# Optimization experiments

Hardware: AMD Instinct MI355X
Metric: run time of the kernel (lower is better)

The kernel has to match this reference:

```python
import jax, jax.numpy as jnp
import numpy as np

N_NODES = 50000


def gcn_conv(x, W, b, src, dst, n):
    """PyG GCNConv: add self-loops, sym-normalize, linear, scatter-add."""
    loop = jnp.arange(n, dtype=src.dtype)
    s = jnp.concatenate([src, loop])  # [E+N]
    d = jnp.concatenate([dst, loop])
    deg = jax.ops.segment_sum(jnp.ones_like(s, dtype=x.dtype), d, num_segments=n)
    dinv = jnp.where(deg > 0, jax.lax.rsqrt(deg), 0.0)  # deg^-1/2
    norm = dinv[s] * dinv[d]  # [E+N]
    h = x @ W  # [N, out] dense GEMM first (in >= out)
    msg = h[s] * norm[:, None]  # gather + scale
    out = jax.ops.segment_sum(msg, d, num_segments=n)  # scatter-add
    return out + b


def setup_inputs() -> dict:
    key = jax.random.key(0)
    k1, k2, k3, k4, k5, k6, k7, k8 = jax.random.split(key, 8)
    in_c, hid_c, out_c = 512, 128, 64
    n, e, l = N_NODES, 800000, 100000
    x = jax.random.normal(k1, (n, in_c), dtype=jnp.float32)
    edge_index = jax.random.randint(k2, (2, e), 0, n, dtype=jnp.int64)
    edge_label_index = jax.random.randint(k3, (2, l), 0, n, dtype=jnp.int64)
    # Glorot-ish init for weights, zeros for biases (PyG default bias=zeros)
    W1 = jax.random.normal(k4, (in_c, hid_c), dtype=jnp.float32) / np.sqrt(in_c)
    b1 = jnp.zeros((hid_c,), dtype=jnp.float32)
    W2 = jax.random.normal(k5, (hid_c, out_c), dtype=jnp.float32) / np.sqrt(hid_c)
    b2 = jnp.zeros((out_c,), dtype=jnp.float32)
    return {"x": x, "edge_index": edge_index, "edge_label_index": edge_label_index,
            "W1": W1, "b1": b1, "W2": W2, "b2": b2}


def reference(x, edge_index, edge_label_index, W1, b1, W2, b2):
    n = x.shape[0]
    src, dst = edge_index[0], edge_index[1]
    z = jax.nn.relu(gcn_conv(x, W1, b1, src, dst, n))
    z = gcn_conv(z, W2, b2, src, dst, n)
    es, ed = edge_label_index[0], edge_label_index[1]
    return jnp.sum(z[es] * z[ed], axis=-1).reshape(-1)
```

## Files before the change

kernel.cpp:

```cpp
#include <hip/hip_runtime.h>

#define IN_C  512
#define HID_C 128
#define OUT_C 64

using short8 = __attribute__((ext_vector_type(8))) short;
using floatx4 = __attribute__((ext_vector_type(4))) float;

__device__ inline unsigned short f2bf(float f) {
    unsigned u = __builtin_bit_cast(unsigned, f);
    u += 0x7FFFu + ((u >> 16) & 1u);
    return (unsigned short)(u >> 16);
}
__device__ inline float bf2f(unsigned short h) {
    unsigned u = ((unsigned)h) << 16;
    return __builtin_bit_cast(float, u);
}

__global__ void k_zero_int(int* __restrict__ p, int n) {
    int i = blockIdx.x * blockDim.x + threadIdx.x;
    if (i < n) p[i] = 0;
}

__global__ void k_count(const int* __restrict__ dst, int* __restrict__ cnt, int e) {
    int i = blockIdx.x * blockDim.x + threadIdx.x;
    if (i < e) atomicAdd(&cnt[dst[i]], 1);
}

__global__ void k_dinv(const int* __restrict__ cnt, float* __restrict__ dinv, int n) {
    int i = blockIdx.x * blockDim.x + threadIdx.x;
    if (i < n) dinv[i] = rsqrtf(1.0f + (float)cnt[i]);
}

__global__ void k_blocksum(const int* __restrict__ cnt, int* __restrict__ bsum, int n) {
    __shared__ int sdata[256];
    int t = threadIdx.x;
    int i = blockIdx.x * 256 + t;
    sdata[t] = (i < n) ? cnt[i] : 0;
    __syncthreads();
    for (int s = 128; s > 0; s >>= 1) {
        if (t < s) sdata[t] += sdata[t + s];
        __syncthreads();
    }
    if (t == 0) bsum[blockIdx.x] = sdata[0];
}

__global__ void k_scanpartials(int* __restrict__ bsum, int nb) {
    __shared__ int sdata[256];
    int t = threadIdx.x;
    int orig = (t < nb) ? bsum[t] : 0;
    sdata[t] = orig;
    __syncthreads();
    for (int off = 1; off < 256; off <<= 1) {
        int v = (t >= off) ? sdata[t - off] : 0;
        __syncthreads();
        sdata[t] += v;
        __syncthreads();
    }
    if (t < nb) bsum[t] = sdata[t] - orig;
}

__global__ void k_scanfinal(const int* __restrict__ cnt, const int* __restrict__ bsum_ex,
                            int* __restrict__ row_ptr, int n, int e_total) {
    __shared__ int sdata[256];
    int t = threadIdx.x;
    int i = blockIdx.x * 256 + t;
    int orig = (i < n) ? cnt[i] : 0;
    sdata[t] = orig;
    __syncthreads();
    for (int off = 1; off < 256; off <<= 1) {
        int v = (t >= off) ? sdata[t - off] : 0;
        __syncthreads();
        sdata[t] += v;
        __syncthreads();
    }
    if (i < n) row_ptr[i] = sdata[t] - orig + bsum_ex[blockIdx.x];
    if (i == 0) row_ptr[n] = e_total;
}

__global__ void k_fill(const int* __restrict__ src, const int* __restrict__ dst,
                       const int* __restrict__ row_ptr, int* __restrict__ cur,
                       int* __restrict__ col, int e) {
    int i = blockIdx.x * blockDim.x + threadIdx.x;
    if (i < e) {
        int d = dst[i];
        int pos = atomicAdd(&cur[d], 1);
        col[row_ptr[d] + pos] = src[i];
    }
}

__global__ void k_prep_w(const float* __restrict__ W, unsigned short* __restrict__ hi,
                         unsigned short* __restrict__ lo, int K, int N) {
    int i = blockIdx.x * blockDim.x + threadIdx.x;
    if (i >= K * N) return;
    int k = i / N, n = i % N;
    float v = W[i];
    unsigned short h = f2bf(v);
    float r = v - bf2f(h);
    hi[(long)n * K + k] = h;
    lo[(long)n * K + k] = f2bf(r);
}

template <int K, int NPW>
__global__ __launch_bounds__(256) void k_gemm_mfma(
    const float* __restrict__ A, const unsigned short* __restrict__ Bt_hi,
    const unsigned short* __restrict__ Bt_lo, const float* __restrict__ dinv,
    float* __restrict__ Hs, int M) {
    constexpr int N = 64 * NPW;
    constexpr int LDA = 72;
    constexpr int NT = K / 64;
    __shared__ __align__(16) unsigned short As_hi[2][64 * LDA];
    __shared__ __align__(16) unsigned short As_lo[2][64 * LDA];

    const int tid = threadIdx.x;
    const int w = tid >> 6;
    const int lane = tid & 63;
    const int m = lane & 15;
    const int quad = lane >> 4;
    const int m0 = blockIdx.x * 64;

    const int srow = tid >> 4;
    const int skk = (tid & 15) << 2;

    floatx4 acc[4][NPW];
#pragma unroll
    for (int mi = 0; mi < 4; ++mi)
#pragma unroll
        for (int ni = 0; ni < NPW; ++ni) acc[mi][ni] = (floatx4){0.f, 0.f, 0.f, 0.f};

    float4 pf[4];
#pragma unroll
    for (int i = 0; i < 4; ++i) {
        int gm = m0 + srow + 16 * i;
        pf[i] = make_float4(0.f, 0.f, 0.f, 0.f);
        if (gm < M) pf[i] = *(const float4*)&A[(long)gm * K + skk];
    }
#pragma unroll
    for (int i = 0; i < 4; ++i) {
        ushort4 h, l;
        h.x = f2bf(pf[i].x); l.x = f2bf(pf[i].x - bf2f(h.x));
        h.y = f2bf(pf[i].y); l.y = f2bf(pf[i].y - bf2f(h.y));
        h.z = f2bf(pf[i].z); l.z = f2bf(pf[i].z - bf2f(h.z));
        h.w = f2bf(pf[i].w); l.w = f2bf(pf[i].w - bf2f(h.w));
        int off = (srow + 16 * i) * LDA + skk;
        *(ushort4*)&As_hi[0][off] = h;
        *(ushort4*)&As_lo[0][off] = l;
    }

    for (int t = 0; t < NT; ++t) {
        __syncthreads();
        const int buf = t & 1;
        if (t + 1 < NT) {
#pragma unroll
            for (int i = 0; i < 4; ++i) {
                int gm = m0 + srow + 16 * i;
                pf[i] = make_float4(0.f, 0.f, 0.f, 0.f);
                if (gm < M) pf[i] = *(const float4*)&A[(long)gm * K + (t + 1) * 64 + skk];
            }
        }
#pragma unroll
        for (int s = 0; s < 2; ++s) {
            short8 ah[4], al[4];
#pragma unroll
            for (int mi = 0; mi < 4; ++mi) {
                int off = (mi * 16 + m) * LDA + s * 32 + quad * 8;
                ah[mi] = *(const short8*)&As_hi[buf][off];
                al[mi] = *(const short8*)&As_lo[buf][off];
            }
#pragma unroll
            for (int ni = 0; ni < NPW; ++ni) {
                int n = (w * NPW + ni) * 16 + m;
                long boff = (long)n * K + t * 64 + s * 32 + quad * 8;
                short8 bh = *(const short8*)&Bt_hi[boff];
                short8 bl = *(const short8*)&Bt_lo[boff];
#pragma unroll
                for (int mi = 0; mi < 4; ++mi) {
                    acc[mi][ni] = __builtin_amdgcn_mfma_f32_16x16x32_bf16(ah[mi], bh, acc[mi][ni], 0, 0, 0);
                    acc[mi][ni] = __builtin_amdgcn_mfma_f32_16x16x32_bf16(ah[mi], bl, acc[mi][ni], 0, 0, 0);
                    acc[mi][ni] = __builtin_amdgcn_mfma_f32_16x16x32_bf16(al[mi], bh, acc[mi][ni], 0, 0, 0);
                }
            }
        }
        if (t + 1 < NT) {
#pragma unroll
            for (int i = 0; i < 4; ++i) {
                ushort4 h, l;
                h.x = f2bf(pf[i].x); l.x = f2bf(pf[i].x - bf2f(h.x));
                h.y = f2bf(pf[i].y); l.y = f2bf(pf[i].y - bf2f(h.y));
                h.z = f2bf(pf[i].z); l.z = f2bf(pf[i].z - bf2f(h.z));
                h.w = f2bf(pf[i].w); l.w = f2bf(pf[i].w - bf2f(h.w));
                int off = (srow + 16 * i) * LDA + skk;
                *(ushort4*)&As_hi[buf ^ 1][off] = h;
                *(ushort4*)&As_lo[buf ^ 1][off] = l;
            }
        }
    }

#pragma unroll
    for (int mi = 0; mi < 4; ++mi) {
#pragma unroll
        for (int r = 0; r < 4; ++r) {
            int row = m0 + mi * 16 + quad * 4 + r;
            if (row < M) {
                float dv = dinv[row];
#pragma unroll
                for (int ni = 0; ni < NPW; ++ni) {
                    int n = (w * NPW + ni) * 16 + m;
                    Hs[(long)row * N + n] = acc[mi][ni][r] * dv;
                }
            }
        }
    }
}

__global__ __launch_bounds__(256) void k_agg1(
    const float* __restrict__ h, const int* __restrict__ row_ptr,
    const int* __restrict__ col, const float* __restrict__ dinv,
    const float* __restrict__ bias, float* __restrict__ z, int n) {
    int node = blockIdx.x * 4 + (threadIdx.x >> 6);
    node = __builtin_amdgcn_readfirstlane(node);
    if (node >= n) return;
    int lane = threadIdx.x & 63;
    const float2* hp = (const float2*)h;
    float2 acc = hp[(long)node * 64 + lane];
    int rs = row_ptr[node], re = row_ptr[node + 1];
    int j = rs;
    for (; j + 4 <= re; j += 4) {
        int s0 = col[j], s1 = col[j + 1], s2 = col[j + 2], s3 = col[j + 3];
        float2 v0 = hp[(long)s0 * 64 + lane];
        float2 v1 = hp[(long)s1 * 64 + lane];
        float2 v2 = hp[(long)s2 * 64 + lane];
        float2 v3 = hp[(long)s3 * 64 + lane];
        acc.x += v0.x + v1.x + v2.x + v3.x;
        acc.y += v0.y + v1.y + v2.y + v3.y;
    }
    for (; j < re; ++j) {
        int s = col[j];
        float2 v = hp[(long)s * 64 + lane];
        acc.x += v.x;
        acc.y += v.y;
    }
    float dv = dinv[node];
    float2 b = ((const float2*)bias)[lane];
    acc.x = fmaxf(fmaf(acc.x, dv, b.x), 0.f);
    acc.y = fmaxf(fmaf(acc.y, dv, b.y), 0.f);
    ((float2*)z)[(long)node * 64 + lane] = acc;
}

__global__ __launch_bounds__(256) void k_agg2(
    const float* __restrict__ h, const int* __restrict__ row_ptr,
    const int* __restrict__ col, const float* __restrict__ dinv,
    const float* __restrict__ bias, float* __restrict__ z, int n) {
    int node = blockIdx.x * 4 + (threadIdx.x >> 6);
    node = __builtin_amdgcn_readfirstlane(node);
    if (node >= n) return;
    int lane = threadIdx.x & 63;
    float acc = h[(long)node * 64 + lane];
    int rs = row_ptr[node], re = row_ptr[node + 1];
    int j = rs;
    for (; j + 4 <= re; j += 4) {
        int s0 = col[j], s1 = col[j + 1], s2 = col[j + 2], s3 = col[j + 3];
        acc += h[(long)s0 * 64 + lane] + h[(long)s1 * 64 + lane] +
               h[(long)s2 * 64 + lane] + h[(long)s3 * 64 + lane];
    }
    for (; j < re; ++j) acc += h[(long)col[j] * 64 + lane];
    z[(long)node * 64 + lane] = fmaf(acc, dinv[node], bias[lane]);
}

__global__ void k_dot(const float* __restrict__ z2, const int* __restrict__ es,
                      const int* __restrict__ ed, float* __restrict__ out, int L) {
    int gid = blockIdx.x * blockDim.x + threadIdx.x;
    int wid = gid >> 6;
    int lane = threadIdx.x & 63;
    if (wid >= L) return;
    int a = es[wid], b = ed[wid];
    float v = z2[(long)a * OUT_C + lane] * z2[(long)b * OUT_C + lane];
#pragma unroll
    for (int off = 32; off > 0; off >>= 1) v += __shfl_down(v, off);
    if (lane == 0) out[wid] = v;
}

extern "C" void kernel_launch(void* const* d_in, const int* in_sizes, int n_in,
                              void* d_out, int out_size, void* d_ws, size_t ws_size,
                              hipStream_t stream) {
    const float* x = (const float*)d_in[0];
    const int* ei = (const int*)d_in[1];
    const int* eli = (const int*)d_in[2];
    const float* W1 = (const float*)d_in[3];
    const float* b1 = (const float*)d_in[4];
    const float* W2 = (const float*)d_in[5];
    const float* b2 = (const float*)d_in[6];
    float* out = (float*)d_out;

    const int N = in_sizes[0] / IN_C;
    const int E = in_sizes[1] / 2;
    const int L = in_sizes[2] / 2;
    const int* src = ei;
    const int* dst = ei + E;
    const int* es = eli;
    const int* ed = eli + L;

    const int Npad = (N + 63) & ~63;
    const int Epad = (E + 3) & ~3;

    int* cnt = (int*)d_ws;
    int* cur = cnt + Npad;
    int* row_ptr = cur + Npad;
    int* bsum = row_ptr + Npad + 64;
    int* col = bsum + 256;
    float* dinv = (float*)(col + Epad);
    float* h1s = dinv + Npad;
    float* z1 = h1s + (long)N * HID_C;
    float* h2s = h1s;
    float* z2 = h1s + (long)N * OUT_C;
    unsigned short* wt1_hi = (unsigned short*)(z1 + (long)N * HID_C);
    unsigned short* wt1_lo = wt1_hi + IN_C * HID_C;
    unsigned short* wt2_hi = wt1_lo + IN_C * HID_C;
    unsigned short* wt2_lo = wt2_hi + HID_C * OUT_C;

    const int TPB = 256;
    const int nb = (N + 255) / 256;

    k_prep_w<<<(IN_C * HID_C + TPB - 1) / TPB, TPB, 0, stream>>>(W1, wt1_hi, wt1_lo, IN_C, HID_C);
    k_prep_w<<<(HID_C * OUT_C + TPB - 1) / TPB, TPB, 0, stream>>>(W2, wt2_hi, wt2_lo, HID_C, OUT_C);

    k_zero_int<<<(2 * Npad + TPB - 1) / TPB, TPB, 0, stream>>>(cnt, 2 * Npad);
    k_count<<<(E + TPB - 1) / TPB, TPB, 0, stream>>>(dst, cnt, E);
    k_dinv<<<(N + TPB - 1) / TPB, TPB, 0, stream>>>(cnt, dinv, N);
    k_blocksum<<<nb, 256, 0, stream>>>(cnt, bsum, N);
    k_scanpartials<<<1, 256, 0, stream>>>(bsum, nb);
    k_scanfinal<<<nb, 256, 0, stream>>>(cnt, bsum, row_ptr, N, E);
    k_fill<<<(E + TPB - 1) / TPB, TPB, 0, stream>>>(src, dst, row_ptr, cur, col, E);

    k_gemm_mfma<IN_C, 2><<<(N + 63) / 64, 256, 0, stream>>>(x, wt1_hi, wt1_lo, dinv, h1s, N);
    k_agg1<<<(N + 3) / 4, 256, 0, stream>>>(h1s, row_ptr, col, dinv, b1, z1, N);

    k_gemm_mfma<HID_C, 1><<<(N + 63) / 64, 256, 0, stream>>>(z1, wt2_hi, wt2_lo, dinv, h2s, N);
    k_agg2<<<(N + 3) / 4, 256, 0, stream>>>(h2s, row_ptr, col, dinv, b2, z2, N);

    k_dot<<<((long)L * 64 + TPB - 1) / TPB, TPB, 0, stream>>>(z2, es, ed, out, L);
}
```

Baseline: 405.0 us.

## Store GEMM outputs in fp16, vectorize aggregation, and fuse small setup kernels

The GEMM now writes the dinv-scaled hidden features as fp16, halving the bytes gathered by both aggregation kernels. The aggregation kernels are rewritten so each quarter-wave walks a quarter of the neighbour list with 16-byte loads, then combines partials across quarter-waves with shuffles. Several setup kernels are merged: both weight-prep launches become one, dinv is folded into the block-sum kernel, and the fill step reuses the count array via atomicSub, which drops the separate cursor buffer and halves the zeroing. The link-dot kernel handles four edges per wavefront with float4 loads. The fp16 intermediates lose some precision and range, and the atomicSub fill reverses the order of entries within each row.

```diff
diff --git a/kernel.cpp b/kernel.cpp
--- a/kernel.cpp
+++ b/kernel.cpp
@@ -16,6 +16,13 @@
     unsigned u = ((unsigned)h) << 16;
     return __builtin_bit_cast(float, u);
 }
+__device__ inline unsigned short f2h(float f) {
+    _Float16 h = (_Float16)f;
+    return __builtin_bit_cast(unsigned short, h);
+}
+__device__ inline float h2f(unsigned v) {
+    return (float)__builtin_bit_cast(_Float16, (unsigned short)v);
+}
 
 __global__ void k_zero_int(int* __restrict__ p, int n) {
     int i = blockIdx.x * blockDim.x + threadIdx.x;
@@ -27,16 +34,14 @@
     if (i < e) atomicAdd(&cnt[dst[i]], 1);
 }
 
-__global__ void k_dinv(const int* __restrict__ cnt, float* __restrict__ dinv, int n) {
-    int i = blockIdx.x * blockDim.x + threadIdx.x;
-    if (i < n) dinv[i] = rsqrtf(1.0f + (float)cnt[i]);
-}
-
-__global__ void k_blocksum(const int* __restrict__ cnt, int* __restrict__ bsum, int n) {
+__global__ void k_blocksum_dinv(const int* __restrict__ cnt, int* __restrict__ bsum,
+                                float* __restrict__ dinv, int n) {
     __shared__ int sdata[256];
     int t = threadIdx.x;
     int i = blockIdx.x * 256 + t;
-    sdata[t] = (i < n) ? cnt[i] : 0;
+    int c = (i < n) ? cnt[i] : 0;
+    if (i < n) dinv[i] = rsqrtf(1.0f + (float)c);
+    sdata[t] = c;
     __syncthreads();
     for (int s = 128; s > 0; s >>= 1) {
         if (t < s) sdata[t] += sdata[t + s];
@@ -79,33 +84,41 @@
 }
 
 __global__ void k_fill(const int* __restrict__ src, const int* __restrict__ dst,
-                       const int* __restrict__ row_ptr, int* __restrict__ cur,
+                       const int* __restrict__ row_ptr, int* __restrict__ cnt,
                        int* __restrict__ col, int e) {
     int i = blockIdx.x * blockDim.x + threadIdx.x;
     if (i < e) {
         int d = dst[i];
-        int pos = atomicAdd(&cur[d], 1);
+        int pos = atomicSub(&cnt[d], 1) - 1;
         col[row_ptr[d] + pos] = src[i];
     }
 }
 
-__global__ void k_prep_w(const float* __restrict__ W, unsigned short* __restrict__ hi,
-                         unsigned short* __restrict__ lo, int K, int N) {
+__global__ void k_prep_w2(const float* __restrict__ W1, unsigned short* __restrict__ hi1,
+                          unsigned short* __restrict__ lo1, const float* __restrict__ W2,
+                          unsigned short* __restrict__ hi2, unsigned short* __restrict__ lo2) {
     int i = blockIdx.x * blockDim.x + threadIdx.x;
-    if (i >= K * N) return;
-    int k = i / N, n = i % N;
-    float v = W[i];
-    unsigned short h = f2bf(v);
-    float r = v - bf2f(h);
-    hi[(long)n * K + k] = h;
-    lo[(long)n * K + k] = f2bf(r);
+    if (i < IN_C * HID_C) {
+        int k = i / HID_C, n = i % HID_C;
+        float v = W1[i];
+        unsigned short h = f2bf(v);
+        hi1[(long)n * IN_C + k] = h;
+        lo1[(long)n * IN_C + k] = f2bf(v - bf2f(h));
+    } else if (i < IN_C * HID_C + HID_C * OUT_C) {
+        int j = i - IN_C * HID_C;
+        int k = j / OUT_C, n = j % OUT_C;
+        float v = W2[j];
+        unsigned short h = f2bf(v);
+        hi2[(long)n * HID_C + k] = h;
+        lo2[(long)n * HID_C + k] = f2bf(v - bf2f(h));
+    }
 }
 
 template <int K, int NPW>
 __global__ __launch_bounds__(256) void k_gemm_mfma(
     const float* __restrict__ A, const unsigned short* __restrict__ Bt_hi,
     const unsigned short* __restrict__ Bt_lo, const float* __restrict__ dinv,
-    float* __restrict__ Hs, int M) {
+    unsigned short* __restrict__ Hs, int M) {
     constexpr int N = 64 * NPW;
     constexpr int LDA = 72;
     constexpr int NT = K / 64;
@@ -206,7 +219,7 @@
 #pragma unroll
                 for (int ni = 0; ni < NPW; ++ni) {
                     int n = (w * NPW + ni) * 16 + m;
-                    Hs[(long)row * N + n] = acc[mi][ni][r] * dv;
+                    Hs[(long)row * N + n] = f2h(acc[mi][ni][r] * dv);
                 }
             }
         }
@@ -214,57 +227,99 @@
 }
 
 __global__ __launch_bounds__(256) void k_agg1(
-    const float* __restrict__ h, const int* __restrict__ row_ptr,
+    const unsigned short* __restrict__ h, const int* __restrict__ row_ptr,
     const int* __restrict__ col, const float* __restrict__ dinv,
     const float* __restrict__ bias, float* __restrict__ z, int n) {
     int node = blockIdx.x * 4 + (threadIdx.x >> 6);
     node = __builtin_amdgcn_readfirstlane(node);
     if (node >= n) return;
     int lane = threadIdx.x & 63;
-    const float2* hp = (const float2*)h;
-    float2 acc = hp[(long)node * 64 + lane];
+    int q = lane >> 4, li = lane & 15;
+    const uint4* hp = (const uint4*)h;
+    float acc[8] = {0.f, 0.f, 0.f, 0.f, 0.f, 0.f, 0.f, 0.f};
+    auto addrow = [&](uint4 v) {
+        acc[0] += h2f(v.x); acc[1] += h2f(v.x >> 16);
+        acc[2] += h2f(v.y); acc[3] += h2f(v.y >> 16);
+        acc[4] += h2f(v.z); acc[5] += h2f(v.z >> 16);
+        acc[6] += h2f(v.w); acc[7] += h2f(v.w >> 16);
+    };
+    if (q == 0) addrow(hp[(long)node * 16 + li]);
     int rs = row_ptr[node], re = row_ptr[node + 1];
-    int j = rs;
-    for (; j + 4 <= re; j += 4) {
-        int s0 = col[j], s1 = col[j + 1], s2 = col[j + 2], s3 = col[j + 3];
-        float2 v0 = hp[(long)s0 * 64 + lane];
-        float2 v1 = hp[(long)s1 * 64 + lane];
-        float2 v2 = hp[(long)s2 * 64 + lane];
-        float2 v3 = hp[(long)s3 * 64 + lane];
-        acc.x += v0.x + v1.x + v2.x + v3.x;
-        acc.y += v0.y + v1.y + v2.y + v3.y;
-    }
-    for (; j < re; ++j) {
-        int s = col[j];
-        float2 v = hp[(long)s * 64 + lane];
-        acc.x += v.x;
-        acc.y += v.y;
-    }
-    float dv = dinv[node];
-    float2 b = ((const float2*)bias)[lane];
-    acc.x = fmaxf(fmaf(acc.x, dv, b.x), 0.f);
-    acc.y = fmaxf(fmaf(acc.y, dv, b.y), 0.f);
-    ((float2*)z)[(long)node * 64 + lane] = acc;
+    int j = rs + q;
+    for (; j + 12 < re; j += 16) {
+        int s0 = col[j], s1 = col[j + 4], s2 = col[j + 8], s3 = col[j + 12];
+        uint4 v0 = hp[(long)s0 * 16 + li];
+        uint4 v1 = hp[(long)s1 * 16 + li];
+        uint4 v2 = hp[(long)s2 * 16 + li];
+        uint4 v3 = hp[(long)s3 * 16 + li];
+        addrow(v0); addrow(v1); addrow(v2); addrow(v3);
+    }
+    for (; j < re; j += 4) addrow(hp[(long)col[j] * 16 + li]);
+#pragma unroll
+    for (int k = 0; k < 8; ++k) {
+        acc[k] += __shfl_xor(acc[k], 16);
+        acc[k] += __shfl_xor(acc[k], 32);
+    }
+    if (q == 0) {
+        float dv = dinv[node];
+        const float4* bp = (const float4*)bias;
+        float4 b0 = bp[li * 2], b1 = bp[li * 2 + 1];
+        float4 o0, o1;
+        o0.x = fmaxf(fmaf(acc[0], dv, b0.x), 0.f);
+        o0.y = fmaxf(fmaf(acc[1], dv, b0.y), 0.f);
+        o0.z = fmaxf(fmaf(acc[2], dv, b0.z), 0.f);
+        o0.w = fmaxf(fmaf(acc[3], dv, b0.w), 0.f);
+        o1.x = fmaxf(fmaf(acc[4], dv, b1.x), 0.f);
+        o1.y = fmaxf(fmaf(acc[5], dv, b1.y), 0.f);
+        o1.z = fmaxf(fmaf(acc[6], dv, b1.z), 0.f);
+        o1.w = fmaxf(fmaf(acc[7], dv, b1.w), 0.f);
+        ((float4*)z)[(long)node * 32 + li * 2] = o0;
+        ((float4*)z)[(long)node * 32 + li * 2 + 1] = o1;
+    }
 }
 
 __global__ __launch_bounds__(256) void k_agg2(
-    const float* __restrict__ h, const int* __restrict__ row_ptr,
+    const unsigned short* __restrict__ h, const int* __restrict__ row_ptr,
     const int* __restrict__ col, const float* __restrict__ dinv,
     const float* __restrict__ bias, float* __restrict__ z, int n) {
     int node = blockIdx.x * 4 + (threadIdx.x >> 6);
     node = __builtin_amdgcn_readfirstlane(node);
     if (node >= n) return;
     int lane = threadIdx.x & 63;
-    float acc = h[(long)node * 64 + lane];
+    int q = lane >> 4, li = lane & 15;
+    const uint2* hp = (const uint2*)h;
+    float acc[4] = {0.f, 0.f, 0.f, 0.f};
+    auto addrow = [&](uint2 v) {
+        acc[0] += h2f(v.x); acc[1] += h2f(v.x >> 16);
+        acc[2] += h2f(v.y); acc[3] += h2f(v.y >> 16);
+    };
+    if (q == 0) addrow(hp[(long)node * 16 + li]);
     int rs = row_ptr[node], re = row_ptr[node + 1];
-    int j = rs;
-    for (; j + 4 <= re; j += 4) {
-        int s0 = col[j], s1 = col[j + 1], s2 = col[j + 2], s3 = col[j + 3];
-        acc += h[(long)s0 * 64 + lane] + h[(long)s1 * 64 + lane] +
-               h[(long)s2 * 64 + lane] + h[(long)s3 * 64 + lane];
-    }
-    for (; j < re; ++j) acc += h[(long)col[j] * 64 + lane];
-    z[(long)node * 64 + lane] = fmaf(acc, dinv[node], bias[lane]);
+    int j = rs + q;
+    for (; j + 12 < re; j += 16) {
+        int s0 = col[j], s1 = col[j + 4], s2 = col[j + 8], s3 = col[j + 12];
+        uint2 v0 = hp[(long)s0 * 16 + li];
+        uint2 v1 = hp[(long)s1 * 16 + li];
+        uint2 v2 = hp[(long)s2 * 16 + li];
+        uint2 v3 = hp[(long)s3 * 16 + li];
+        addrow(v0); addrow(v1); addrow(v2); addrow(v3);
+    }
+    for (; j < re; j += 4) addrow(hp[(long)col[j] * 16 + li]);
+#pragma unroll
+    for (int k = 0; k < 4; ++k) {
+        acc[k] += __shfl_xor(acc[k], 16);
+        acc[k] += __shfl_xor(acc[k], 32);
+    }
+    if (q == 0) {
+        float dv = dinv[node];
+        float4 b = ((const float4*)bias)[li];
+        float4 o;
+        o.x = fmaf(acc[0], dv, b.x);
+        o.y = fmaf(acc[1], dv, b.y);
+        o.z = fmaf(acc[2], dv, b.z);
+        o.w = fmaf(acc[3], dv, b.w);
+        ((float4*)z)[(long)node * 16 + li] = o;
+    }
 }
 
 __global__ void k_dot(const float* __restrict__ z2, const int* __restrict__ es,
@@ -272,12 +327,17 @@
     int gid = blockIdx.x * blockDim.x + threadIdx.x;
     int wid = gid >> 6;
     int lane = threadIdx.x & 63;
-    if (wid >= L) return;
-    int a = es[wid], b = ed[wid];
-    float v = z2[(long)a * OUT_C + lane] * z2[(long)b * OUT_C + lane];
-#pragma unroll
-    for (int off = 32; off > 0; off >>= 1) v += __shfl_down(v, off);
-    if (lane == 0) out[wid] = v;
+    int q = lane >> 4, li = lane & 15;
+    int e = wid * 4 + q;
+    if (e >= L) return;
+    int a = es[e], b = ed[e];
+    const float4* zp = (const float4*)z2;
+    float4 za = zp[(long)a * 16 + li];
+    float4 zb = zp[(long)b * 16 + li];
+    float v = za.x * zb.x + za.y * zb.y + za.z * zb.z + za.w * zb.w;
+#pragma unroll
+    for (int off = 8; off > 0; off >>= 1) v += __shfl_xor(v, off);
+    if (li == 0) out[e] = v;
 }
 
 extern "C" void kernel_launch(void* const* d_in, const int* in_sizes, int n_in,
@@ -304,16 +364,15 @@
     const int Epad = (E + 3) & ~3;
 
     int* cnt = (int*)d_ws;
-    int* cur = cnt + Npad;
-    int* row_ptr = cur + Npad;
+    int* row_ptr = cnt + Npad;
     int* bsum = row_ptr + Npad + 64;
     int* col = bsum + 256;
     float* dinv = (float*)(col + Epad);
-    float* h1s = dinv + Npad;
-    float* z1 = h1s + (long)N * HID_C;
-    float* h2s = h1s;
-    float* z2 = h1s + (long)N * OUT_C;
-    unsigned short* wt1_hi = (unsigned short*)(z1 + (long)N * HID_C);
+    unsigned short* h1s = (unsigned short*)(dinv + Npad);
+    float* z1 = (float*)(h1s + (long)N * HID_C);
+    unsigned short* h2s = h1s;
+    float* z2 = z1 + (long)N * HID_C;
+    unsigned short* wt1_hi = (unsigned short*)(z2 + (long)N * OUT_C);
     unsigned short* wt1_lo = wt1_hi + IN_C * HID_C;
     unsigned short* wt2_hi = wt1_lo + IN_C * HID_C;
     unsigned short* wt2_lo = wt2_hi + HID_C * OUT_C;
@@ -321,16 +380,15 @@
     const int TPB = 256;
     const int nb = (N + 255) / 256;
 
-    k_prep_w<<<(IN_C * HID_C + TPB - 1) / TPB, TPB, 0, stream>>>(W1, wt1_hi, wt1_lo, IN_C, HID_C);
-    k_prep_w<<<(HID_C * OUT_C + TPB - 1) / TPB, TPB, 0, stream>>>(W2, wt2_hi, wt2_lo, HID_C, OUT_C);
-
-    k_zero_int<<<(2 * Npad + TPB - 1) / TPB, TPB, 0, stream>>>(cnt, 2 * Npad);
+    const int PW = IN_C * HID_C + HID_C * OUT_C;
+    k_prep_w2<<<(PW + TPB - 1) / TPB, TPB, 0, stream>>>(W1, wt1_hi, wt1_lo, W2, wt2_hi, wt2_lo);
+
+    k_zero_int<<<(Npad + TPB - 1) / TPB, TPB, 0, stream>>>(cnt, Npad);
     k_count<<<(E + TPB - 1) / TPB, TPB, 0, stream>>>(dst, cnt, E);
-    k_dinv<<<(N + TPB - 1) / TPB, TPB, 0, stream>>>(cnt, dinv, N);
-    k_blocksum<<<nb, 256, 0, stream>>>(cnt, bsum, N);
+    k_blocksum_dinv<<<nb, 256, 0, stream>>>(cnt, bsum, dinv, N);
     k_scanpartials<<<1, 256, 0, stream>>>(bsum, nb);
     k_scanfinal<<<nb, 256, 0, stream>>>(cnt, bsum, row_ptr, N, E);
-    k_fill<<<(E + TPB - 1) / TPB, TPB, 0, stream>>>(src, dst, row_ptr, cur, col, E);
+    k_fill<<<(E + TPB - 1) / TPB, TPB, 0, stream>>>(src, dst, row_ptr, cnt, col, E);
 
     k_gemm_mfma<IN_C, 2><<<(N + 63) / 64, 256, 0, stream>>>(x, wt1_hi, wt1_lo, dinv, h1s, N);
     k_agg1<<<(N + 3) / 4, 256, 0, stream>>>(h1s, row_ptr, col, dinv, b1, z1, N);
@@ -338,5 +396,5 @@
     k_gemm_mfma<HID_C, 1><<<(N + 63) / 64, 256, 0, stream>>>(z1, wt2_hi, wt2_lo, dinv, h2s, N);
     k_agg2<<<(N + 3) / 4, 256, 0, stream>>>(h2s, row_ptr, col, dinv, b2, z2, N);
 
-    k_dot<<<((long)L * 64 + TPB - 1) / TPB, TPB, 0, stream>>>(z2, es, ed, out, L);
-}
+    k_dot<<<((long)((L + 3) / 4) * 64 + TPB - 1) / TPB, TPB, 0, stream>>>(z2, es, ed, out, L);
+}
```

Measured after the change: 367.6 us. 9.2% less time.
